# Kernel tuning notes

Hardware: AMD Instinct MI355X
Metric: run time of the kernel (lower is better)

## Reference

```python
import jax, jax.numpy as jnp
import numpy as np

DIM = 512
NUM_HEADS = 16
RANK = 4
HEAD_DIM = DIM // NUM_HEADS
SCALE = HEAD_DIM ** -0.5
B_, N, NW = 2048, 49, 64


def setup_inputs() -> dict:
    key = jax.random.key(0)
    ks = jax.random.split(key, 9)
    x = jax.random.normal(ks[0], (B_, N, DIM), dtype=jnp.float32)
    mask = jax.random.normal(ks[1], (NW, N, N), dtype=jnp.float32)
    # qkv base linear (torch Linear stores weight [out,in])
    W_qkv = jax.random.normal(ks[2], (3 * DIM, DIM), dtype=jnp.float32) * (DIM ** -0.5)
    b_qkv = jax.random.normal(ks[3], (3 * DIM,), dtype=jnp.float32) * 0.02
    # LoRA down [rank, dim], up [3*dim, rank] (zero-init in module; use small random for non-trivial math)
    A_down = jax.random.normal(ks[4], (RANK, DIM), dtype=jnp.float32) * 0.02
    B_up = jax.random.normal(ks[5], (3 * DIM, RANK), dtype=jnp.float32) * 0.02
    W_proj = jax.random.normal(ks[6], (DIM, DIM), dtype=jnp.float32) * (DIM ** -0.5)
    b_proj = jax.random.normal(ks[7], (DIM,), dtype=jnp.float32) * 0.02
    return {"x": x, "mask": mask, "W_qkv": W_qkv, "b_qkv": b_qkv,
            "A_down": A_down, "B_up": B_up, "W_proj": W_proj, "b_proj": b_proj}


def reference(x, mask, W_qkv, b_qkv, A_down, B_up, W_proj, b_proj):
    Bw, n, C = x.shape
    H, hd = NUM_HEADS, HEAD_DIM
    # LoRA-augmented QKV projection: base linear + up(down(x))
    qkv = x @ W_qkv.T + b_qkv + (x @ A_down.T) @ B_up.T          # [B_, N, 3C]
    qkv = qkv.reshape(Bw, n, 3, H, hd)
    q = qkv[:, :, 0].transpose(0, 2, 1, 3)                        # [B_, H, N, hd]
    k = qkv[:, :, 1].transpose(0, 2, 1, 3)
    v = qkv[:, :, 2].transpose(0, 2, 1, 3)
    attn = jnp.einsum('bhnd,bhmd->bhnm', q, k) * SCALE            # [B_, H, N, N]
    nW = mask.shape[0]
    attn = attn.reshape(Bw // nW, nW, H, n, n) + mask[None, :, None]
    attn = attn.reshape(Bw, H, n, n)
    attn = jax.nn.softmax(attn, axis=-1)
    out = jnp.einsum('bhnm,bhmd->bhnd', attn, v)                  # [B_, H, N, hd]
    out = out.transpose(0, 2, 1, 3).reshape(Bw, n, C)
    return out @ W_proj.T + b_proj
```

## Files before the change

kernel.cpp:

```cpp
#include <hip/hip_runtime.h>
#include <stdint.h>

typedef __attribute__((ext_vector_type(4))) float f32x4;
typedef __attribute__((ext_vector_type(8))) __bf16 bf16x8;
typedef __attribute__((ext_vector_type(4))) unsigned int u32x4;
typedef __attribute__((ext_vector_type(4))) unsigned short u16x4;

#define TOK 49
#define NHEAD 16
#define HDIM 32
#define CDIM 512
#define NB 2048
#define MTOT (NB * TOK)
#define ATT_SCALE 0.17677669529663687f

__device__ __forceinline__ unsigned short f2bf(float f) {
  uint32_t u = __builtin_bit_cast(uint32_t, f);
  u += 0x7FFFu + ((u >> 16) & 1u);
  return (unsigned short)(u >> 16);
}

__device__ __forceinline__ void gl_lds16(const void* g, const void* lds) {
  __builtin_amdgcn_global_load_lds(
      (__attribute__((address_space(1))) void*)(uintptr_t)g,
      (__attribute__((address_space(3))) void*)(uint32_t)(uintptr_t)lds,
      16, 0, 0);
}

__device__ __forceinline__ f32x4 mfma16(bf16x8 a, bf16x8 b, f32x4 c) {
  return __builtin_amdgcn_mfma_f32_16x16x32_bf16(a, b, c, 0, 0, 0);
}

__global__ __launch_bounds__(256) void k_prep_weff(
    const float* __restrict__ Wqkv, const float* __restrict__ Bup,
    const float* __restrict__ Adown, unsigned short* __restrict__ weff) {
  int idx = blockIdx.x * 256 + threadIdx.x;
  if (idx >= 3 * CDIM * CDIM) return;
  int o = idx >> 9, i = idx & 511;
  float v = Wqkv[idx];
#pragma unroll
  for (int r = 0; r < 4; r++) v += Bup[o * 4 + r] * Adown[r * 512 + i];
  weff[idx] = f2bf(v);
}

__global__ __launch_bounds__(256) void k_conv4(
    const float* __restrict__ src, unsigned short* __restrict__ dst, int n4) {
  for (int i = blockIdx.x * blockDim.x + threadIdx.x; i < n4;
       i += gridDim.x * blockDim.x) {
    f32x4 v = *(const f32x4*)(src + (size_t)i * 4);
    u16x4 o;
    o[0] = f2bf(v[0]); o[1] = f2bf(v[1]); o[2] = f2bf(v[2]); o[3] = f2bf(v[3]);
    *(u16x4*)(dst + (size_t)i * 4) = o;
  }
}

template <int NT, bool SPLIT>
__global__ __launch_bounds__(256, 3) void k_gemm128(
    const unsigned short* __restrict__ A, const unsigned short* __restrict__ Bw,
    const float* __restrict__ bias,
    unsigned short* __restrict__ qo, unsigned short* __restrict__ ko,
    unsigned short* __restrict__ vo, float* __restrict__ fo) {
  __shared__ __attribute__((aligned(16))) unsigned short smem[24576];
  const int t = threadIdx.x;
  const int l = t & 63;
  const int l15 = l & 15, lq = l >> 4;
  const int w = t >> 6;
  const int wr = w >> 1, wc = w & 1;
  const int bid = blockIdx.x;
  const int lb = (bid & 7) * ((int)gridDim.x >> 3) + (bid >> 3);
  const int mt = lb / NT, nt = lb % NT;
  const size_t m0 = (size_t)mt * 128;
  const int n0 = nt * 128;

  auto stage = [&](int kt, int bb) {
    unsigned short* dA = smem + bb * 4096;
    unsigned short* dB = smem + 12288 + bb * 4096;
#pragma unroll
    for (int q = 0; q < 2; ++q) {
      const int li = q * 256 + t;
      const int row = li >> 2, sl = li & 3;
      const int kof = kt * 32 + ((sl ^ ((row >> 1) & 3)) << 3);
      gl_lds16(A + (m0 + row) * CDIM + kof, &dA[li * 8]);
    }
#pragma unroll
    for (int q = 0; q < 2; ++q) {
      const int li = q * 256 + t;
      const int row = li >> 2, sl = li & 3;
      const int kof = kt * 32 + ((sl ^ ((row >> 1) & 3)) << 3);
      gl_lds16(Bw + (size_t)(n0 + row) * CDIM + kof, &dB[li * 8]);
    }
  };

  f32x4 acc[4][4] = {};
  stage(0, 0);
  stage(1, 1);
  for (int kt = 0; kt < 16; ++kt) {
    const int cur = kt % 3;
    if (kt < 15) {
      asm volatile("s_waitcnt vmcnt(4)" ::: "memory");
    } else {
      asm volatile("s_waitcnt vmcnt(0)" ::: "memory");
    }
    __builtin_amdgcn_s_barrier();
    asm volatile("" ::: "memory");
    if (kt < 14) stage(kt + 2, (kt + 2) % 3);
    const unsigned short* bufA = smem + cur * 4096;
    const unsigned short* bufB = smem + 12288 + cur * 4096;
    bf16x8 af[4], bfv[4];
#pragma unroll
    for (int c = 0; c < 4; ++c) {
      const int r = wc * 64 + c * 16 + l15;
      bfv[c] = __builtin_bit_cast(
          bf16x8, *(const u32x4*)&bufB[r * 32 + ((lq ^ ((r >> 1) & 3)) << 3)]);
    }
#pragma unroll
    for (int f = 0; f < 4; ++f) {
      const int r = wr * 64 + f * 16 + l15;
      af[f] = __builtin_bit_cast(
          bf16x8, *(const u32x4*)&bufA[r * 32 + ((lq ^ ((r >> 1) & 3)) << 3)]);
    }
    __builtin_amdgcn_s_setprio(1);
#pragma unroll
    for (int f = 0; f < 4; ++f) {
#pragma unroll
      for (int c = 0; c < 4; ++c) acc[f][c] = mfma16(af[f], bfv[c], acc[f][c]);
    }
    __builtin_amdgcn_s_setprio(0);
    asm volatile("" ::: "memory");
  }

  __syncthreads();
  if constexpr (SPLIT) {
    unsigned short* ep = smem + w * 4096;
#pragma unroll
    for (int J = 0; J < 4; ++J) {
      const int colb = n0 + wc * 64 + J * 16 + l15;
      const float bv = bias[colb];
      const int sl0 = J * 2 + (l15 >> 3);
#pragma unroll
      for (int I = 0; I < 4; ++I) {
#pragma unroll
        for (int r = 0; r < 4; ++r) {
          const int row = I * 16 + lq * 4 + r;
          ep[row * 64 + ((sl0 ^ (row & 7)) << 3) + (l15 & 7)] =
              f2bf(acc[I][J][r] + bv);
        }
      }
    }
    asm volatile("s_waitcnt lgkmcnt(0)" ::: "memory");
#pragma unroll
    for (int rnd = 0; rnd < 8; ++rnd) {
      const int sub = rnd * 16 + (l >> 2);
      const int mloc = sub >> 1, hd2 = sub & 1;
      const int colh = n0 + wc * 64 + hd2 * 32;
      const int which = colh >> 9;
      const int hh = (colh >> 5) & 15;
      unsigned short* dst = which == 0 ? qo : (which == 1 ? ko : vo);
      const uint32_t mg = (uint32_t)(m0 + wr * 64 + mloc);
      const uint32_t bw_ = mg / 49u;
      const uint32_t nn = mg - bw_ * 49u;
      const int sl = hd2 * 4 + (l & 3);
      u32x4 v = *(const u32x4*)&ep[mloc * 64 + ((sl ^ (mloc & 7)) << 3)];
      *(u32x4*)&dst[((size_t)(bw_ * 16u + hh) * 49u + nn) * 32u + (l & 3) * 8] =
          v;
    }
  } else {
    float* ep32 = (float*)smem + w * 2048;
#pragma unroll
    for (int ch = 0; ch < 2; ++ch) {
#pragma unroll
      for (int J = 0; J < 4; ++J) {
        const int colb = n0 + wc * 64 + J * 16 + l15;
        const float bv = bias[colb];
        const int sl0 = J * 4 + (l15 >> 2);
#pragma unroll
        for (int Ii = 0; Ii < 2; ++Ii) {
#pragma unroll
          for (int r = 0; r < 4; ++r) {
            const int row = Ii * 16 + lq * 4 + r;
            ep32[row * 64 + ((sl0 ^ (row & 7)) << 2) + (l15 & 3)] =
                acc[ch * 2 + Ii][J][r] + bv;
          }
        }
      }
      asm volatile("s_waitcnt lgkmcnt(0)" ::: "memory");
#pragma unroll
      for (int rnd = 0; rnd < 8; ++rnd) {
        const int row = rnd * 4 + (l >> 4);
        const int sl = l & 15;
        f32x4 v = *(const f32x4*)&ep32[row * 64 + ((sl ^ (row & 7)) << 2)];
        const size_t mg = m0 + wr * 64 + ch * 32 + row;
        *(f32x4*)&fo[mg * CDIM + n0 + wc * 64 + (l & 15) * 4] = v;
      }
      asm volatile("s_waitcnt lgkmcnt(0)" ::: "memory");
      asm volatile("" ::: "memory");
    }
  }
}

__global__ __launch_bounds__(256) void k_attn(
    const unsigned short* __restrict__ qb, const unsigned short* __restrict__ kb,
    const unsigned short* __restrict__ vb, const float* __restrict__ mask,
    unsigned short* __restrict__ ao) {
  __shared__ __attribute__((aligned(16))) unsigned short sP[4][64 * 64];
  __shared__ __attribute__((aligned(16))) unsigned short sV[4][32 * 64];
  const int t = threadIdx.x;
  const int l = t & 63, w = t >> 6;
  const int l15 = l & 15, lq = l >> 4;
  const int pair = blockIdx.x * 4 + w;
  const int b = pair >> 4, h = pair & 15;
  const size_t base = (size_t)pair * (TOK * HDIM);
  unsigned short* P = sP[w];
  unsigned short* Vt = sV[w];

  bf16x8 qf[4], kf[4];
#pragma unroll
  for (int i = 0; i < 4; i++)
    qf[i] = __builtin_bit_cast(
        bf16x8, *(const u32x4*)(qb + base + (size_t)(i * 16 + l15) * 32 + lq * 8));
#pragma unroll
  for (int i = 0; i < 4; i++)
    kf[i] = __builtin_bit_cast(
        bf16x8, *(const u32x4*)(kb + base + (size_t)(i * 16 + l15) * 32 + lq * 8));
  u32x4 vr[4];
#pragma unroll
  for (int j = 0; j < 4; j++)
    vr[j] = *(const u32x4*)(vb + base + (size_t)l * 32 + j * 8);

  f32x4 s[4][4];
  __builtin_amdgcn_s_setprio(1);
#pragma unroll
  for (int i = 0; i < 4; i++) {
#pragma unroll
    for (int j = 0; j < 4; j++) s[i][j] = mfma16(qf[i], kf[j], (f32x4)0.0f);
  }
  __builtin_amdgcn_s_setprio(0);

  const bool vok = (l < TOK);
  const int tsl = ((l >> 3) & 7);
  const int tlo = l & 7;
#pragma unroll
  for (int j = 0; j < 4; j++) {
#pragma unroll
    for (int c = 0; c < 4; c++) {
      uint32_t u = vr[j][c];
      int d0 = j * 8 + c * 2;
      Vt[(d0 + 0) * 64 + ((tsl ^ ((d0 + 0) & 7)) << 3) + tlo] =
          vok ? (unsigned short)(u & 0xFFFFu) : (unsigned short)0;
      Vt[(d0 + 1) * 64 + ((tsl ^ ((d0 + 1) & 7)) << 3) + tlo] =
          vok ? (unsigned short)(u >> 16) : (unsigned short)0;
    }
  }

  const float* mrow = mask + (size_t)(b & 63) * (TOK * TOK);
#pragma unroll
  for (int i = 0; i < 4; i++) {
#pragma unroll
    for (int r = 0; r < 4; r++) {
      int row = i * 16 + lq * 4 + r;
#pragma unroll
      for (int j = 0; j < 4; j++) {
        int col = j * 16 + l15;
        float xv = s[i][j][r] * ATT_SCALE;
        if (col < TOK) {
          if (row < TOK) xv += mrow[row * TOK + col];
        } else {
          xv = -1e30f;
        }
        s[i][j][r] = xv;
      }
    }
  }

  float rinv[4][4];
#pragma unroll
  for (int i = 0; i < 4; i++) {
#pragma unroll
    for (int r = 0; r < 4; r++) {
      float m = fmaxf(fmaxf(s[i][0][r], s[i][1][r]), fmaxf(s[i][2][r], s[i][3][r]));
      m = fmaxf(m, __shfl_xor(m, 1));
      m = fmaxf(m, __shfl_xor(m, 2));
      m = fmaxf(m, __shfl_xor(m, 4));
      m = fmaxf(m, __shfl_xor(m, 8));
      float sum = 0.f;
      int row = i * 16 + lq * 4 + r;
#pragma unroll
      for (int j = 0; j < 4; j++) {
        float p = __expf(s[i][j][r] - m);
        sum += p;
        P[row * 64 + (((j * 2 + (l15 >> 3)) ^ (row & 7)) << 3) + (l15 & 7)] =
            f2bf(p);
      }
      sum += __shfl_xor(sum, 1);
      sum += __shfl_xor(sum, 2);
      sum += __shfl_xor(sum, 4);
      sum += __shfl_xor(sum, 8);
      rinv[i][r] = 1.0f / sum;
    }
  }

  asm volatile("s_waitcnt lgkmcnt(0)" ::: "memory");
  __builtin_amdgcn_sched_barrier(0);

  f32x4 o[4][2] = {};
#pragma unroll
  for (int ks = 0; ks < 2; ks++) {
    bf16x8 pa[4], vf[2];
#pragma unroll
    for (int i = 0; i < 4; i++)
      pa[i] = __builtin_bit_cast(
          bf16x8,
          *(const u32x4*)&P[(i * 16 + l15) * 64 + (((lq + ks * 4) ^ (l15 & 7)) << 3)]);
#pragma unroll
    for (int j = 0; j < 2; j++)
      vf[j] = __builtin_bit_cast(
          bf16x8,
          *(const u32x4*)&Vt[(j * 16 + l15) * 64 + (((lq + ks * 4) ^ (l15 & 7)) << 3)]);
    __builtin_amdgcn_s_setprio(1);
#pragma unroll
    for (int i = 0; i < 4; i++) {
#pragma unroll
      for (int j = 0; j < 2; j++) o[i][j] = mfma16(pa[i], vf[j], o[i][j]);
    }
    __builtin_amdgcn_s_setprio(0);
  }

#pragma unroll
  for (int i = 0; i < 4; i++) {
#pragma unroll
    for (int r = 0; r < 4; r++) {
      int row = i * 16 + lq * 4 + r;
      if (row < TOK) {
        float inv = rinv[i][r];
        size_t obase = ((size_t)b * TOK + row) * CDIM + h * HDIM;
#pragma unroll
        for (int j = 0; j < 2; j++)
          ao[obase + j * 16 + l15] = f2bf(o[i][j][r] * inv);
      }
    }
  }
}

extern "C" void kernel_launch(void* const* d_in, const int* in_sizes, int n_in,
                              void* d_out, int out_size, void* d_ws,
                              size_t ws_size, hipStream_t stream) {
  const float* x = (const float*)d_in[0];
  const float* mask = (const float*)d_in[1];
  const float* Wqkv = (const float*)d_in[2];
  const float* bqkv = (const float*)d_in[3];
  const float* Adown = (const float*)d_in[4];
  const float* Bup = (const float*)d_in[5];
  const float* Wproj = (const float*)d_in[6];
  const float* bproj = (const float*)d_in[7];
  float* out = (float*)d_out;
  char* ws = (char*)d_ws;

  size_t off = 0;
  auto alloc = [&](size_t bytes) {
    size_t o = off;
    off += (bytes + 255) & ~(size_t)255;
    return o;
  };
  const size_t qkv_elems = (size_t)NB * NHEAD * TOK * HDIM;
  unsigned short* weff = (unsigned short*)(ws + alloc((size_t)3 * CDIM * CDIM * 2));
  unsigned short* wpb = (unsigned short*)(ws + alloc((size_t)CDIM * CDIM * 2));
  unsigned short* qb = (unsigned short*)(ws + alloc(qkv_elems * 2 + 4096));
  unsigned short* kb = (unsigned short*)(ws + alloc(qkv_elems * 2 + 4096));
  unsigned short* vb = (unsigned short*)(ws + alloc(qkv_elems * 2 + 4096));
  unsigned short* xb = (unsigned short*)(ws + alloc((size_t)MTOT * CDIM * 2));
  unsigned short* ao = xb;

  k_prep_weff<<<(3 * CDIM * CDIM + 255) / 256, 256, 0, stream>>>(Wqkv, Bup,
                                                                 Adown, weff);
  k_conv4<<<256, 256, 0, stream>>>(Wproj, wpb, CDIM * CDIM / 4);
  k_conv4<<<2048, 256, 0, stream>>>(x, xb, MTOT * CDIM / 4);
  k_gemm128<12, true><<<(MTOT / 128) * 12, 256, 0, stream>>>(
      xb, weff, bqkv, qb, kb, vb, nullptr);
  k_attn<<<NB * NHEAD / 4, 256, 0, stream>>>(qb, kb, vb, mask, ao);
  k_gemm128<4, false><<<(MTOT / 128) * 4, 256, 0, stream>>>(
      ao, wpb, bproj, nullptr, nullptr, nullptr, out);
}
```

Measured before the change: 559.6 us.

## Widen GEMM tiles to 128x256 and use native bf16 conversion

Both GEMMs now use 128x256 output tiles, with each wave computing a 64x128 sub-tile. This halves the grid size and doubles how often each loaded A tile is reused, so less A traffic is refetched per output. The price is more LDS, more accumulator registers and lower occupancy (launch bounds drop to 2 blocks per SM), plus reworked epilogues with an extra barrier. The f2bf helper also switches to the compiler's native __bf16 cast instead of manual rounding.

After: 541.5 us. 1.03x faster.

```diff
diff --git a/kernel.cpp b/kernel.cpp
--- a/kernel.cpp
+++ b/kernel.cpp
@@ -15,9 +15,7 @@
 #define ATT_SCALE 0.17677669529663687f
 
 __device__ __forceinline__ unsigned short f2bf(float f) {
-  uint32_t u = __builtin_bit_cast(uint32_t, f);
-  u += 0x7FFFu + ((u >> 16) & 1u);
-  return (unsigned short)(u >> 16);
+  return __builtin_bit_cast(unsigned short, (__bf16)f);
 }
 
 __device__ __forceinline__ void gl_lds16(const void* g, const void* lds) {
@@ -55,12 +53,12 @@
 }
 
 template <int NT, bool SPLIT>
-__global__ __launch_bounds__(256, 3) void k_gemm128(
+__global__ __launch_bounds__(256, 2) void k_gemmW(
     const unsigned short* __restrict__ A, const unsigned short* __restrict__ Bw,
     const float* __restrict__ bias,
     unsigned short* __restrict__ qo, unsigned short* __restrict__ ko,
     unsigned short* __restrict__ vo, float* __restrict__ fo) {
-  __shared__ __attribute__((aligned(16))) unsigned short smem[24576];
+  __shared__ __attribute__((aligned(16))) unsigned short smem[36864];
   const int t = threadIdx.x;
   const int l = t & 63;
   const int l15 = l & 15, lq = l >> 4;
@@ -70,34 +68,35 @@
   const int lb = (bid & 7) * ((int)gridDim.x >> 3) + (bid >> 3);
   const int mt = lb / NT, nt = lb % NT;
   const size_t m0 = (size_t)mt * 128;
-  const int n0 = nt * 128;
+  const int n0 = nt * 256;
 
   auto stage = [&](int kt, int bb) {
     unsigned short* dA = smem + bb * 4096;
-    unsigned short* dB = smem + 12288 + bb * 4096;
 #pragma unroll
     for (int q = 0; q < 2; ++q) {
       const int li = q * 256 + t;
       const int row = li >> 2, sl = li & 3;
-      const int kof = kt * 32 + ((sl ^ ((row >> 1) & 3)) << 3);
-      gl_lds16(A + (m0 + row) * CDIM + kof, &dA[li * 8]);
-    }
-#pragma unroll
-    for (int q = 0; q < 2; ++q) {
+      gl_lds16(A + (m0 + row) * CDIM + kt * 32 + ((sl ^ ((row >> 1) & 3)) << 3),
+               &dA[li * 8]);
+    }
+    unsigned short* dB = smem + 12288 + bb * 8192;
+#pragma unroll
+    for (int q = 0; q < 4; ++q) {
       const int li = q * 256 + t;
       const int row = li >> 2, sl = li & 3;
-      const int kof = kt * 32 + ((sl ^ ((row >> 1) & 3)) << 3);
-      gl_lds16(Bw + (size_t)(n0 + row) * CDIM + kof, &dB[li * 8]);
+      gl_lds16(Bw + (size_t)(n0 + row) * CDIM + kt * 32 +
+                   ((sl ^ ((row >> 1) & 3)) << 3),
+               &dB[li * 8]);
     }
   };
 
-  f32x4 acc[4][4] = {};
+  f32x4 acc[4][8] = {};
   stage(0, 0);
   stage(1, 1);
   for (int kt = 0; kt < 16; ++kt) {
     const int cur = kt % 3;
     if (kt < 15) {
-      asm volatile("s_waitcnt vmcnt(4)" ::: "memory");
+      asm volatile("s_waitcnt vmcnt(6)" ::: "memory");
     } else {
       asm volatile("s_waitcnt vmcnt(0)" ::: "memory");
     }
@@ -105,25 +104,25 @@
     asm volatile("" ::: "memory");
     if (kt < 14) stage(kt + 2, (kt + 2) % 3);
     const unsigned short* bufA = smem + cur * 4096;
-    const unsigned short* bufB = smem + 12288 + cur * 4096;
-    bf16x8 af[4], bfv[4];
-#pragma unroll
-    for (int c = 0; c < 4; ++c) {
-      const int r = wc * 64 + c * 16 + l15;
-      bfv[c] = __builtin_bit_cast(
-          bf16x8, *(const u32x4*)&bufB[r * 32 + ((lq ^ ((r >> 1) & 3)) << 3)]);
-    }
+    const unsigned short* bufB = smem + 12288 + cur * 8192;
+    bf16x8 af[4], bfv[8];
 #pragma unroll
     for (int f = 0; f < 4; ++f) {
       const int r = wr * 64 + f * 16 + l15;
       af[f] = __builtin_bit_cast(
           bf16x8, *(const u32x4*)&bufA[r * 32 + ((lq ^ ((r >> 1) & 3)) << 3)]);
     }
+#pragma unroll
+    for (int c = 0; c < 8; ++c) {
+      const int r = wc * 128 + c * 16 + l15;
+      bfv[c] = __builtin_bit_cast(
+          bf16x8, *(const u32x4*)&bufB[r * 32 + ((lq ^ ((r >> 1) & 3)) << 3)]);
+    }
     __builtin_amdgcn_s_setprio(1);
 #pragma unroll
     for (int f = 0; f < 4; ++f) {
 #pragma unroll
-      for (int c = 0; c < 4; ++c) acc[f][c] = mfma16(af[f], bfv[c], acc[f][c]);
+      for (int c = 0; c < 8; ++c) acc[f][c] = mfma16(af[f], bfv[c], acc[f][c]);
     }
     __builtin_amdgcn_s_setprio(0);
     asm volatile("" ::: "memory");
@@ -131,10 +130,10 @@
 
   __syncthreads();
   if constexpr (SPLIT) {
-    unsigned short* ep = smem + w * 4096;
-#pragma unroll
-    for (int J = 0; J < 4; ++J) {
-      const int colb = n0 + wc * 64 + J * 16 + l15;
+    unsigned short* ep = smem + w * 8192;
+#pragma unroll
+    for (int J = 0; J < 8; ++J) {
+      const int colb = n0 + wc * 128 + J * 16 + l15;
       const float bv = bias[colb];
       const int sl0 = J * 2 + (l15 >> 3);
 #pragma unroll
@@ -142,55 +141,56 @@
 #pragma unroll
         for (int r = 0; r < 4; ++r) {
           const int row = I * 16 + lq * 4 + r;
-          ep[row * 64 + ((sl0 ^ (row & 7)) << 3) + (l15 & 7)] =
+          ep[row * 128 + ((sl0 ^ (row & 7)) << 3) + (l15 & 7)] =
               f2bf(acc[I][J][r] + bv);
         }
       }
     }
     asm volatile("s_waitcnt lgkmcnt(0)" ::: "memory");
-#pragma unroll
-    for (int rnd = 0; rnd < 8; ++rnd) {
+    __builtin_amdgcn_s_barrier();
+#pragma unroll
+    for (int rnd = 0; rnd < 16; ++rnd) {
       const int sub = rnd * 16 + (l >> 2);
-      const int mloc = sub >> 1, hd2 = sub & 1;
-      const int colh = n0 + wc * 64 + hd2 * 32;
+      const int mloc = sub >> 2, hd = sub & 3;
+      const int colh = n0 + wc * 128 + hd * 32;
       const int which = colh >> 9;
       const int hh = (colh >> 5) & 15;
       unsigned short* dst = which == 0 ? qo : (which == 1 ? ko : vo);
       const uint32_t mg = (uint32_t)(m0 + wr * 64 + mloc);
       const uint32_t bw_ = mg / 49u;
       const uint32_t nn = mg - bw_ * 49u;
-      const int sl = hd2 * 4 + (l & 3);
-      u32x4 v = *(const u32x4*)&ep[mloc * 64 + ((sl ^ (mloc & 7)) << 3)];
+      const int slot = hd * 4 + (l & 3);
+      u32x4 v = *(const u32x4*)&ep[mloc * 128 + ((slot ^ (mloc & 7)) << 3)];
       *(u32x4*)&dst[((size_t)(bw_ * 16u + hh) * 49u + nn) * 32u + (l & 3) * 8] =
           v;
     }
   } else {
-    float* ep32 = (float*)smem + w * 2048;
+    float* ep32 = (float*)(smem) + w * 4096;
 #pragma unroll
     for (int ch = 0; ch < 2; ++ch) {
 #pragma unroll
-      for (int J = 0; J < 4; ++J) {
-        const int colb = n0 + wc * 64 + J * 16 + l15;
+      for (int J2 = 0; J2 < 4; ++J2) {
+        const int colb = n0 + wc * 128 + ch * 64 + J2 * 16 + l15;
         const float bv = bias[colb];
-        const int sl0 = J * 4 + (l15 >> 2);
-#pragma unroll
-        for (int Ii = 0; Ii < 2; ++Ii) {
+        const int sl0 = J2 * 4 + (l15 >> 2);
+#pragma unroll
+        for (int I = 0; I < 4; ++I) {
 #pragma unroll
           for (int r = 0; r < 4; ++r) {
-            const int row = Ii * 16 + lq * 4 + r;
+            const int row = I * 16 + lq * 4 + r;
             ep32[row * 64 + ((sl0 ^ (row & 7)) << 2) + (l15 & 3)] =
-                acc[ch * 2 + Ii][J][r] + bv;
+                acc[I][ch * 4 + J2][r] + bv;
           }
         }
       }
       asm volatile("s_waitcnt lgkmcnt(0)" ::: "memory");
 #pragma unroll
-      for (int rnd = 0; rnd < 8; ++rnd) {
+      for (int rnd = 0; rnd < 16; ++rnd) {
         const int row = rnd * 4 + (l >> 4);
-        const int sl = l & 15;
-        f32x4 v = *(const f32x4*)&ep32[row * 64 + ((sl ^ (row & 7)) << 2)];
-        const size_t mg = m0 + wr * 64 + ch * 32 + row;
-        *(f32x4*)&fo[mg * CDIM + n0 + wc * 64 + (l & 15) * 4] = v;
+        const int slot = l & 15;
+        f32x4 v = *(const f32x4*)&ep32[row * 64 + ((slot ^ (row & 7)) << 2)];
+        const size_t mg = m0 + wr * 64 + row;
+        *(f32x4*)&fo[mg * CDIM + n0 + wc * 128 + ch * 64 + (l & 15) * 4] = v;
       }
       asm volatile("s_waitcnt lgkmcnt(0)" ::: "memory");
       asm volatile("" ::: "memory");
@@ -374,9 +374,9 @@
                                                                  Adown, weff);
   k_conv4<<<256, 256, 0, stream>>>(Wproj, wpb, CDIM * CDIM / 4);
   k_conv4<<<2048, 256, 0, stream>>>(x, xb, MTOT * CDIM / 4);
-  k_gemm128<12, true><<<(MTOT / 128) * 12, 256, 0, stream>>>(
+  k_gemmW<6, true><<<(MTOT / 128) * 6, 256, 0, stream>>>(
       xb, weff, bqkv, qb, kb, vb, nullptr);
   k_attn<<<NB * NHEAD / 4, 256, 0, stream>>>(qb, kb, vb, mask, ao);
-  k_gemm128<4, false><<<(MTOT / 128) * 4, 256, 0, stream>>>(
+  k_gemmW<2, false><<<(MTOT / 128) * 2, 256, 0, stream>>>(
       ao, wpb, bproj, nullptr, nullptr, nullptr, out);
 }
```
